# Kernel optimization log

Measured on AMD Instinct MI355X. Metric: run time of the kernel, lower is better.

## Reference

```python
import jax, jax.numpy as jnp
import numpy as np

B, N, D, H, S = 32, 8192, 64, 128, 16
ITERS, TAU = 3, 0.1


def _ln(x, g, b):
    m = x.mean(-1, keepdims=True)
    v = ((x - m) ** 2).mean(-1, keepdims=True)
    return (x - m) / jnp.sqrt(v + 1e-5) * g + b


def setup_inputs() -> dict:
    key = jax.random.key(0)
    ks = jax.random.split(key, 20)
    nrm = lambda k, shp, s: jax.random.normal(k, shp, jnp.float32) * s
    return {
        'x': nrm(ks[0], (B, N, D), 1.0),
        'w1': nrm(ks[1], (D, H), D ** -0.5), 'b1': jnp.zeros((H,), jnp.float32),
        'ln1_g': jnp.ones((H,), jnp.float32), 'ln1_b': jnp.zeros((H,), jnp.float32),
        'w2': nrm(ks[2], (H, H), H ** -0.5), 'b2': jnp.zeros((H,), jnp.float32),
        'ln2_g': jnp.ones((H,), jnp.float32), 'ln2_b': jnp.zeros((H,), jnp.float32),
        'slot_mu': nrm(ks[3], (1, S, H), 0.1),
        'gru_wi': nrm(ks[4], (3 * H, H), H ** -0.5), 'gru_wh': nrm(ks[5], (3 * H, H), H ** -0.5),
        'gru_bi': jnp.zeros((3 * H,), jnp.float32), 'gru_bh': jnp.zeros((3 * H,), jnp.float32),
        'mlp_w1': nrm(ks[6], (H, H), H ** -0.5), 'mlp_b1': jnp.zeros((H,), jnp.float32),
        'mlp_w2': nrm(ks[7], (H, H), H ** -0.5), 'mlp_b2': jnp.zeros((H,), jnp.float32),
        'norm_g': jnp.ones((H,), jnp.float32), 'norm_b': jnp.zeros((H,), jnp.float32),
    }


def reference(x, w1, b1, ln1_g, ln1_b, w2, b2, ln2_g, ln2_b, slot_mu,
              gru_wi, gru_wh, gru_bi, gru_bh, mlp_w1, mlp_b1, mlp_w2, mlp_b2,
              norm_g, norm_b):
    Bb = x.shape[0]
    h = jax.nn.gelu(_ln(x @ w1 + b1, ln1_g, ln1_b), approximate=False)
    feats = _ln(h @ w2 + b2, ln2_g, ln2_b)              # [B,N,H]
    slots = jnp.broadcast_to(slot_mu, (Bb, S, H))
    f2 = jnp.sum(feats * feats, -1)                      # [B,N]
    attn = None
    for _ in range(ITERS):
        s2 = jnp.sum(slots * slots, -1)                  # [B,S]
        sf = jnp.einsum('bsh,bnh->bsn', slots, feats)
        dist_sq = -(s2[:, :, None] - 2.0 * sf + f2[:, None, :])  # -||s-f||^2
        attn = jax.nn.softmax(dist_sq / TAU, axis=1)     # softmax over slots
        w = attn / (attn.sum(2, keepdims=True) + 1e-8)
        updates = jnp.einsum('bsn,bnh->bsh', w, feats)
        # GRUCell (PyTorch gate order: r, z, n)
        gi = updates @ gru_wi.T + gru_bi
        gh = slots @ gru_wh.T + gru_bh
        ir, iz, inn = jnp.split(gi, 3, -1)
        hr, hz, hn = jnp.split(gh, 3, -1)
        r = jax.nn.sigmoid(ir + hr)
        z = jax.nn.sigmoid(iz + hz)
        n = jnp.tanh(inn + r * hn)
        new = (1.0 - z) * n + z * slots
        mlp_out = jax.nn.gelu(_ln(new, norm_g, norm_b) @ mlp_w1 + mlp_b1, approximate=False) @ mlp_w2 + mlp_b2
        slots = new + 0.2 * mlp_out
    return (slots, attn)
```

## Files before the change

kernel.cpp:

```cpp
#include <hip/hip_runtime.h>
#include <cstddef>
#include <cstdint>

#define B_ 32
#define N_ 8192
#define D_ 64
#define H_ 128
#define S_ 16
#define L2SCALE 14.426950408889634f

typedef unsigned short ushort_t;
typedef __attribute__((ext_vector_type(8))) short short8;
typedef __attribute__((ext_vector_type(4))) float f32x4;

#define NCHUNK 512
#define NBLK   (N_ / NCHUNK)
#define PSTRIDE 520

#define W1T_STR 72
#define W2T_STR 136

__device__ __forceinline__ float gelu_exact(float x){
    return 0.5f * x * (1.0f + erff(x * 0.70710678118654752f));
}
__device__ __forceinline__ ushort_t f2bf(float f){
    unsigned u = __float_as_uint(f);
    unsigned r = (u + 0x7FFF + ((u >> 16) & 1)) >> 16;
    return (ushort_t)r;
}
__device__ __forceinline__ float bf2f(ushort_t h){
    return __uint_as_float(((unsigned)h) << 16);
}

__global__ __launch_bounds__(256) void gemm1_kernel(
    const float* __restrict__ x, const float* __restrict__ w1, const float* __restrict__ b1,
    const float* __restrict__ ln1g, const float* __restrict__ ln1b,
    ushort_t* __restrict__ h_hi, ushort_t* __restrict__ h_lo)
{
    __shared__ ushort_t w1t_hi[128*W1T_STR];
    __shared__ ushort_t w1t_lo[128*W1T_STR];

    const int tid  = threadIdx.x;
    const int w    = tid >> 6;
    const int l    = tid & 63;
    const int ln   = l & 15;
    const int quad = l >> 4;
    const size_t n0 = (size_t)blockIdx.x * 256;

    for (int i = tid; i < 8192; i += 256){
        int k = i >> 7, hc = i & 127;
        float v = w1[i];
        ushort_t hi = f2bf(v);
        w1t_hi[hc*W1T_STR + k] = hi;
        w1t_lo[hc*W1T_STR + k] = f2bf(v - bf2f(hi));
    }
    __syncthreads();

    for (int tt = 0; tt < 4; ++tt){
        const size_t row = n0 + (size_t)(w*4 + tt)*16 + ln;
        const float* xr = x + row*64;

        short8 bxh[2], bxl[2];
        #pragma unroll
        for (int kc = 0; kc < 2; ++kc){
            float4 a0 = *(const float4*)(xr + kc*32 + quad*8);
            float4 a1 = *(const float4*)(xr + kc*32 + quad*8 + 4);
            float v[8] = {a0.x,a0.y,a0.z,a0.w,a1.x,a1.y,a1.z,a1.w};
            #pragma unroll
            for (int j=0;j<8;++j){
                ushort_t hi = f2bf(v[j]);
                bxh[kc][j] = (short)hi;
                bxl[kc][j] = (short)f2bf(v[j] - bf2f(hi));
            }
        }

        f32x4 acc[8];
        #pragma unroll
        for (int ht=0;ht<8;++ht) acc[ht] = (f32x4){0.f,0.f,0.f,0.f};

        #pragma unroll
        for (int ht = 0; ht < 8; ++ht){
            #pragma unroll
            for (int kc = 0; kc < 2; ++kc){
                short8 ah = *(const short8*)&w1t_hi[(ht*16+ln)*W1T_STR + kc*32 + quad*8];
                short8 al = *(const short8*)&w1t_lo[(ht*16+ln)*W1T_STR + kc*32 + quad*8];
                acc[ht] = __builtin_amdgcn_mfma_f32_16x16x32_bf16(ah, bxh[kc], acc[ht], 0,0,0);
                acc[ht] = __builtin_amdgcn_mfma_f32_16x16x32_bf16(ah, bxl[kc], acc[ht], 0,0,0);
                acc[ht] = __builtin_amdgcn_mfma_f32_16x16x32_bf16(al, bxh[kc], acc[ht], 0,0,0);
            }
        }

        float vals[8][4];
        float s1 = 0.f, sq = 0.f;
        #pragma unroll
        for (int ht=0;ht<8;++ht){
            float bb[4]; *(float4*)bb = *(const float4*)(b1 + ht*16 + quad*4);
            #pragma unroll
            for (int r=0;r<4;++r){
                float v = acc[ht][r] + bb[r];
                vals[ht][r] = v; s1 += v; sq += v*v;
            }
        }
        s1 += __shfl_xor(s1,16); s1 += __shfl_xor(s1,32);
        sq += __shfl_xor(sq,16); sq += __shfl_xor(sq,32);
        float mean = s1 * (1.f/128.f);
        float var  = sq * (1.f/128.f) - mean*mean;
        float rs   = 1.f / sqrtf(var + 1e-5f);

        #pragma unroll
        for (int ht=0;ht<8;++ht){
            float gg[4]; *(float4*)gg = *(const float4*)(ln1g + ht*16 + quad*4);
            float be[4]; *(float4*)be = *(const float4*)(ln1b + ht*16 + quad*4);
            ushort_t oh[4], ol[4];
            #pragma unroll
            for (int r=0;r<4;++r){
                float t  = (vals[ht][r]-mean)*rs*gg[r] + be[r];
                float ge = gelu_exact(t);
                ushort_t hi = f2bf(ge);
                oh[r] = hi;
                ol[r] = f2bf(ge - bf2f(hi));
            }
            size_t off = row*128 + ht*16 + quad*4;
            *(ushort4*)(h_hi + off) = make_ushort4(oh[0],oh[1],oh[2],oh[3]);
            *(ushort4*)(h_lo + off) = make_ushort4(ol[0],ol[1],ol[2],ol[3]);
        }
    }
}

__global__ __launch_bounds__(256) void gemm2_kernel(
    ushort_t* __restrict__ buf_hi, ushort_t* __restrict__ buf_lo,
    const float* __restrict__ w2, const float* __restrict__ b2,
    const float* __restrict__ ln2g, const float* __restrict__ ln2b)
{
    __shared__ ushort_t w2t_hi[128*W2T_STR];
    __shared__ ushort_t w2t_lo[128*W2T_STR];

    const int tid  = threadIdx.x;
    const int w    = tid >> 6;
    const int l    = tid & 63;
    const int ln   = l & 15;
    const int quad = l >> 4;
    const size_t n0 = (size_t)blockIdx.x * 256;

    for (int i = tid; i < 16384; i += 256){
        int k = i >> 7, hc = i & 127;
        float v = w2[i];
        ushort_t hi = f2bf(v);
        w2t_hi[hc*W2T_STR + k] = hi;
        w2t_lo[hc*W2T_STR + k] = f2bf(v - bf2f(hi));
    }
    __syncthreads();

    for (int g = 0; g < 2; ++g){
        size_t row[2];
        row[0] = n0 + (size_t)(w*4 + g*2 + 0)*16 + ln;
        row[1] = n0 + (size_t)(w*4 + g*2 + 1)*16 + ln;

        f32x4 acc[2][8];
        #pragma unroll
        for (int t2=0;t2<2;++t2)
            #pragma unroll
            for (int ht=0;ht<8;++ht) acc[t2][ht] = (f32x4){0.f,0.f,0.f,0.f};

        #pragma unroll
        for (int kc = 0; kc < 4; ++kc){
            short8 bh[2], bl[2];
            #pragma unroll
            for (int t2=0;t2<2;++t2){
                bh[t2] = *(const short8*)(buf_hi + row[t2]*128 + kc*32 + quad*8);
                bl[t2] = *(const short8*)(buf_lo + row[t2]*128 + kc*32 + quad*8);
            }
            #pragma unroll
            for (int ht = 0; ht < 8; ++ht){
                short8 ah = *(const short8*)&w2t_hi[(ht*16+ln)*W2T_STR + kc*32 + quad*8];
                short8 al = *(const short8*)&w2t_lo[(ht*16+ln)*W2T_STR + kc*32 + quad*8];
                #pragma unroll
                for (int t2=0;t2<2;++t2){
                    acc[t2][ht] = __builtin_amdgcn_mfma_f32_16x16x32_bf16(ah, bh[t2], acc[t2][ht], 0,0,0);
                    acc[t2][ht] = __builtin_amdgcn_mfma_f32_16x16x32_bf16(ah, bl[t2], acc[t2][ht], 0,0,0);
                    acc[t2][ht] = __builtin_amdgcn_mfma_f32_16x16x32_bf16(al, bh[t2], acc[t2][ht], 0,0,0);
                }
            }
        }

        #pragma unroll
        for (int t2=0;t2<2;++t2){
            float vals[8][4];
            float s1 = 0.f, sq = 0.f;
            #pragma unroll
            for (int ht=0;ht<8;++ht){
                float bb[4]; *(float4*)bb = *(const float4*)(b2 + ht*16 + quad*4);
                #pragma unroll
                for (int r=0;r<4;++r){
                    float v = acc[t2][ht][r] + bb[r];
                    vals[ht][r] = v; s1 += v; sq += v*v;
                }
            }
            s1 += __shfl_xor(s1,16); s1 += __shfl_xor(s1,32);
            sq += __shfl_xor(sq,16); sq += __shfl_xor(sq,32);
            float mean = s1 * (1.f/128.f);
            float var  = sq * (1.f/128.f) - mean*mean;
            float rs   = 1.f / sqrtf(var + 1e-5f);
            #pragma unroll
            for (int ht=0;ht<8;++ht){
                float gg[4]; *(float4*)gg = *(const float4*)(ln2g + ht*16 + quad*4);
                float be[4]; *(float4*)be = *(const float4*)(ln2b + ht*16 + quad*4);
                ushort_t oh[4], ol[4];
                #pragma unroll
                for (int r=0;r<4;++r){
                    float o = (vals[ht][r]-mean)*rs*gg[r] + be[r];
                    ushort_t hi = f2bf(o);
                    oh[r] = hi;
                    ol[r] = f2bf(o - bf2f(hi));
                }
                size_t off = row[t2]*128 + ht*16 + quad*4;
                *(ushort4*)(buf_hi + off) = make_ushort4(oh[0],oh[1],oh[2],oh[3]);
                *(ushort4*)(buf_lo + off) = make_ushort4(ol[0],ol[1],ol[2],ol[3]);
            }
        }
    }
}

__global__ void init_slots(const float* __restrict__ mu, float* __restrict__ slots){
    int i = blockIdx.x * 256 + threadIdx.x;
    slots[i] = mu[i & 2047];
}

__global__ __launch_bounds__(512, 2) void attn_kernel(
    const ushort_t* __restrict__ f_hi, const ushort_t* __restrict__ f_lo,
    const float* __restrict__ slots,
    float* __restrict__ pn, float* __restrict__ pd,
    float* __restrict__ attn_out, const int write_attn)
{
    __shared__ ushort_t P_hi[16*PSTRIDE];
    __shared__ ushort_t P_lo[16*PSTRIDE];
    __shared__ float    s2buf[16];
    __shared__ float    den_red[16];

    const int tid  = threadIdx.x;
    const int w    = tid >> 6;
    const int l    = tid & 63;
    const int ln   = l & 15;
    const int quad = l >> 4;
    const int b    = blockIdx.x >> 4;
    const int nc   = blockIdx.x & 15;
    const int n0   = nc * NCHUNK;

    if (tid < 16) den_red[tid] = 0.f;

    short8 sa_hi[4], sa_lo[4];
    float q2 = 0.f;
    {
        const float* sp = slots + ((size_t)(b*16 + ln))*128 + quad*8;
        #pragma unroll
        for (int ks=0; ks<4; ++ks){
            float4 v0 = *(const float4*)(sp + ks*32);
            float4 v1 = *(const float4*)(sp + ks*32 + 4);
            float v[8] = {v0.x,v0.y,v0.z,v0.w,v1.x,v1.y,v1.z,v1.w};
            #pragma unroll
            for (int j=0;j<8;++j){
                q2 += v[j]*v[j];
                ushort_t hi = f2bf(v[j]);
                float lo = v[j] - bf2f(hi);
                sa_hi[ks][j] = (short)hi;
                sa_lo[ks][j] = (short)f2bf(lo);
            }
        }
    }
    q2 += __shfl_xor(q2, 16);
    q2 += __shfl_xor(q2, 32);
    if (tid < 16) s2buf[tid] = q2;
    __syncthreads();

    float s2v[4];
    #pragma unroll
    for (int r=0;r<4;++r) s2v[r] = s2buf[quad*4 + r];

    float den_acc[4] = {0.f,0.f,0.f,0.f};
    const size_t fbase = (size_t)b*N_ + n0;

    #pragma unroll
    for (int t2=0; t2<4; ++t2){
        const int t  = w*4 + t2;
        const int nl = t*16 + ln;
        const size_t rowoff = (fbase + nl) * 128;

        short8 fh[4], fl[4];
        #pragma unroll
        for (int ks=0; ks<4; ++ks){
            fh[ks] = *(const short8*)(f_hi + rowoff + ks*32 + quad*8);
            fl[ks] = *(const short8*)(f_lo + rowoff + ks*32 + quad*8);
        }

        f32x4 d = {0.f,0.f,0.f,0.f};
        #pragma unroll
        for (int ks=0;ks<4;++ks) d = __builtin_amdgcn_mfma_f32_16x16x32_bf16(sa_hi[ks], fh[ks], d, 0,0,0);
        #pragma unroll
        for (int ks=0;ks<4;++ks) d = __builtin_amdgcn_mfma_f32_16x16x32_bf16(sa_hi[ks], fl[ks], d, 0,0,0);
        #pragma unroll
        for (int ks=0;ks<4;++ks) d = __builtin_amdgcn_mfma_f32_16x16x32_bf16(sa_lo[ks], fh[ks], d, 0,0,0);

        float L[4];
        #pragma unroll
        for (int r=0;r<4;++r) L[r] = (2.f*d[r] - s2v[r]) * L2SCALE;
        float mx = fmaxf(fmaxf(L[0],L[1]), fmaxf(L[2],L[3]));
        mx = fmaxf(mx, __shfl_xor(mx, 16));
        mx = fmaxf(mx, __shfl_xor(mx, 32));
        float e[4];
        float z = 0.f;
        #pragma unroll
        for (int r=0;r<4;++r){ e[r] = exp2f(L[r] - mx); z += e[r]; }
        z += __shfl_xor(z, 16);
        z += __shfl_xor(z, 32);
        float rz = 1.f / z;
        #pragma unroll
        for (int r=0;r<4;++r){
            float p = e[r] * rz;
            den_acc[r] += p;
            if (write_attn)
                attn_out[((size_t)(b*16 + quad*4 + r))*N_ + n0 + nl] = p;
            ushort_t ph = f2bf(p);
            float plr = p - bf2f(ph);
            P_hi[(quad*4+r)*PSTRIDE + nl] = ph;
            P_lo[(quad*4+r)*PSTRIDE + nl] = f2bf(plr);
        }
    }

    #pragma unroll
    for (int m=1; m<16; m<<=1){
        #pragma unroll
        for (int r=0;r<4;++r) den_acc[r] += __shfl_xor(den_acc[r], m);
    }
    if (ln == 0){
        #pragma unroll
        for (int r=0;r<4;++r) atomicAdd(&den_red[quad*4 + r], den_acc[r]);
    }
    __syncthreads();

    f32x4 dacc = {0.f,0.f,0.f,0.f};
    #pragma unroll 2
    for (int ks=0; ks<16; ++ks){
        short8 pah = *(const short8*)(&P_hi[ln*PSTRIDE + ks*32 + quad*8]);
        short8 pal = *(const short8*)(&P_lo[ln*PSTRIDE + ks*32 + quad*8]);
        short8 fbh, fbl;
        #pragma unroll
        for (int j=0;j<8;++j){
            size_t go = (fbase + (size_t)(ks*32 + quad*8 + j))*128 + w*16 + ln;
            fbh[j] = (short)f_hi[go];
            fbl[j] = (short)f_lo[go];
        }
        dacc = __builtin_amdgcn_mfma_f32_16x16x32_bf16(pah, fbh, dacc, 0,0,0);
        dacc = __builtin_amdgcn_mfma_f32_16x16x32_bf16(pal, fbh, dacc, 0,0,0);
        dacc = __builtin_amdgcn_mfma_f32_16x16x32_bf16(pah, fbl, dacc, 0,0,0);
    }
    {
        float* dst = pn + (size_t)blockIdx.x * 2048;
        #pragma unroll
        for (int r=0;r<4;++r)
            dst[(quad*4+r)*128 + w*16 + ln] = dacc[r];
    }
    if (tid < 16) pd[blockIdx.x*16 + tid] = den_red[tid];
}

__global__ __launch_bounds__(256) void update_kernel(
    const float* __restrict__ pn, const float* __restrict__ pd,
    float* __restrict__ slots,
    const float* __restrict__ gwi, const float* __restrict__ gwh,
    const float* __restrict__ gbi, const float* __restrict__ gbh,
    const float* __restrict__ mw1, const float* __restrict__ mb1,
    const float* __restrict__ mw2, const float* __restrict__ mb2,
    const float* __restrict__ ng, const float* __restrict__ nbv,
    float* __restrict__ out_slots, const int write_out)
{
    __shared__ float us[512], sl[512], gbuf[3072], nbuf[512], lnb[512], qb[512];
    const int tid  = threadIdx.x;
    const int row0 = blockIdx.x * 4;

    for (int i = tid; i < 512; i += 256){
        int r = i >> 7, h = i & 127;
        int grow = row0 + r;
        int bb = grow >> 4, ss = grow & 15;
        float sum = 0.f, dv = 0.f;
        #pragma unroll 4
        for (int c = 0; c < NBLK; ++c)
            sum += pn[((size_t)(bb*NBLK + c))*2048 + ss*128 + h];
        #pragma unroll
        for (int c = 0; c < NBLK; ++c)
            dv += pd[(bb*NBLK + c)*16 + ss];
        us[i] = sum / (dv + 1e-8f);
        sl[i] = slots[(size_t)grow*128 + h];
    }
    __syncthreads();

    for (int idx = tid; idx < 3072; idx += 256){
        int which = idx >= 1536;
        int rem   = idx - which*1536;
        int r     = rem / 384;
        int o     = rem - r*384;
        const float* W   = which ? gwh : gwi;
        const float* bb  = which ? gbh : gbi;
        const float* src = (which ? sl : us) + r*128;
        float a = bb[o];
        const float4* Wr = (const float4*)(W + (size_t)o*128);
        #pragma unroll 8
        for (int k4=0;k4<32;++k4){
            float4 wv = Wr[k4];
            float4 sv = *(const float4*)(src + 4*k4);
            a += sv.x*wv.x + sv.y*wv.y + sv.z*wv.z + sv.w*wv.w;
        }
        gbuf[idx] = a;
    }
    __syncthreads();

    for (int i = tid; i < 512; i += 256){
        int r = i >> 7, h = i & 127;
        float ir  = gbuf[r*384 + h];
        float iz  = gbuf[r*384 + 128 + h];
        float in_ = gbuf[r*384 + 256 + h];
        float hr  = gbuf[1536 + r*384 + h];
        float hz  = gbuf[1536 + r*384 + 128 + h];
        float hn  = gbuf[1536 + r*384 + 256 + h];
        float rg = 1.f/(1.f + expf(-(ir+hr)));
        float zg = 1.f/(1.f + expf(-(iz+hz)));
        float nn = tanhf(in_ + rg*hn);
        nbuf[i] = (1.f - zg)*nn + zg*sl[i];
    }
    __syncthreads();

    {
        int wv = tid >> 6, ll = tid & 63;
        float v0 = nbuf[wv*128 + ll], v1 = nbuf[wv*128 + 64 + ll];
        float s1 = v0 + v1, sq = v0*v0 + v1*v1;
        #pragma unroll
        for (int m=1; m<64; m<<=1){ s1 += __shfl_xor(s1,m); sq += __shfl_xor(sq,m); }
        float mean = s1*(1.f/128.f), var = sq*(1.f/128.f) - mean*mean;
        float rs = 1.f/sqrtf(var + 1e-5f);
        lnb[wv*128 + ll]      = (v0-mean)*rs*ng[ll] + nbv[ll];
        lnb[wv*128 + 64 + ll] = (v1-mean)*rs*ng[64+ll] + nbv[64+ll];
    }
    __syncthreads();

    for (int i = tid; i < 512; i += 256){
        int r = i >> 7, o = i & 127;
        float a = mb1[o];
        const float* lr = lnb + r*128;
        #pragma unroll 8
        for (int k=0;k<128;++k) a += lr[k] * mw1[(size_t)k*128 + o];
        qb[i] = gelu_exact(a);
    }
    __syncthreads();

    for (int i = tid; i < 512; i += 256){
        int r = i >> 7, h = i & 127;
        float a = mb2[h];
        const float* qr = qb + r*128;
        #pragma unroll 8
        for (int k=0;k<128;++k) a += qr[k] * mw2[(size_t)k*128 + h];
        float ov = nbuf[i] + 0.2f*a;
        int grow = row0 + r;
        slots[(size_t)grow*128 + h] = ov;
        if (write_out) out_slots[(size_t)grow*128 + h] = ov;
    }
}

extern "C" void kernel_launch(void* const* d_in, const int* in_sizes, int n_in,
                              void* d_out, int out_size, void* d_ws, size_t ws_size,
                              hipStream_t stream)
{
    const float* x    = (const float*)d_in[0];
    const float* w1   = (const float*)d_in[1];
    const float* b1   = (const float*)d_in[2];
    const float* ln1g = (const float*)d_in[3];
    const float* ln1b = (const float*)d_in[4];
    const float* w2   = (const float*)d_in[5];
    const float* b2   = (const float*)d_in[6];
    const float* ln2g = (const float*)d_in[7];
    const float* ln2b = (const float*)d_in[8];
    const float* smu  = (const float*)d_in[9];
    const float* gwi  = (const float*)d_in[10];
    const float* gwh  = (const float*)d_in[11];
    const float* gbi  = (const float*)d_in[12];
    const float* gbh  = (const float*)d_in[13];
    const float* mw1  = (const float*)d_in[14];
    const float* mb1  = (const float*)d_in[15];
    const float* mw2  = (const float*)d_in[16];
    const float* mb2  = (const float*)d_in[17];
    const float* ng   = (const float*)d_in[18];
    const float* nbv  = (const float*)d_in[19];

    float* out_slots = (float*)d_out;
    float* out_attn  = (float*)d_out + (size_t)B_*S_*H_;

    ushort_t* buf_hi = (ushort_t*)d_ws;
    ushort_t* buf_lo = buf_hi + (size_t)B_*N_*H_;
    float* slots = (float*)(buf_lo + (size_t)B_*N_*H_);
    float* pn    = slots + B_*S_*H_;
    float* pd    = pn + (size_t)(B_*NBLK)*2048;

    gemm1_kernel<<<dim3(1024), dim3(256), 0, stream>>>(
        x, w1, b1, ln1g, ln1b, buf_hi, buf_lo);
    gemm2_kernel<<<dim3(1024), dim3(256), 0, stream>>>(
        buf_hi, buf_lo, w2, b2, ln2g, ln2b);
    init_slots<<<dim3(256), dim3(256), 0, stream>>>(smu, slots);

    for (int it = 0; it < 3; ++it){
        attn_kernel<<<dim3(B_*NBLK), dim3(512), 0, stream>>>(
            buf_hi, buf_lo, slots, pn, pd, out_attn, (it==2) ? 1 : 0);
        update_kernel<<<dim3(128), dim3(256), 0, stream>>>(
            pn, pd, slots, gwi, gwh, gbi, gbh, mw1, mb1, mw2, mb2, ng, nbv,
            out_slots, (it==2) ? 1 : 0);
    }
}
```

Before: 658.7 us.

## Halve per-block work in all kernels and use fast GELU/exp approximations

Halves the rows handled by each block in the gemm1 and gemm2 kernels and doubles their grid size. Shrinks the attention chunk to 256 tokens with 256-thread blocks, so each wave now computes two output column tiles. Replaces exact erf-based GELU with an Abramowitz-Stegun polynomial using __expf, and uses __expf in the GRU sigmoids. The intent is more blocks in flight and cheaper transcendental math. In exchange, each smaller block repeats the weight-staging prologue, more partials must be reduced, and precision is lowered slightly.

```diff
diff --git a/kernel.cpp b/kernel.cpp
--- a/kernel.cpp
+++ b/kernel.cpp
@@ -13,15 +13,22 @@
 typedef __attribute__((ext_vector_type(8))) short short8;
 typedef __attribute__((ext_vector_type(4))) float f32x4;
 
-#define NCHUNK 512
+#define NCHUNK 256
 #define NBLK   (N_ / NCHUNK)
-#define PSTRIDE 520
+#define PSTRIDE 264
 
 #define W1T_STR 72
 #define W2T_STR 136
 
-__device__ __forceinline__ float gelu_exact(float x){
-    return 0.5f * x * (1.0f + erff(x * 0.70710678118654752f));
+__device__ __forceinline__ float gelu_fast(float x){
+    float z = fabsf(x) * 0.70710678118654752f;
+    float t = 1.0f / fmaf(0.3275911f, z, 1.0f);
+    float p = t*(0.254829592f + t*(-0.284496736f + t*(1.421413741f +
+              t*(-1.453152027f + t*1.061405429f))));
+    float e = __expf(-z*z);
+    float erf_abs = 1.0f - p*e;
+    float er = copysignf(erf_abs, x);
+    return 0.5f * x * (1.0f + er);
 }
 __device__ __forceinline__ ushort_t f2bf(float f){
     unsigned u = __float_as_uint(f);
@@ -45,7 +52,7 @@
     const int l    = tid & 63;
     const int ln   = l & 15;
     const int quad = l >> 4;
-    const size_t n0 = (size_t)blockIdx.x * 256;
+    const size_t n0 = (size_t)blockIdx.x * 128;
 
     for (int i = tid; i < 8192; i += 256){
         int k = i >> 7, hc = i & 127;
@@ -56,8 +63,8 @@
     }
     __syncthreads();
 
-    for (int tt = 0; tt < 4; ++tt){
-        const size_t row = n0 + (size_t)(w*4 + tt)*16 + ln;
+    for (int tt = 0; tt < 2; ++tt){
+        const size_t row = n0 + (size_t)(w*2 + tt)*16 + ln;
         const float* xr = x + row*64;
 
         short8 bxh[2], bxl[2];
@@ -115,7 +122,7 @@
             #pragma unroll
             for (int r=0;r<4;++r){
                 float t  = (vals[ht][r]-mean)*rs*gg[r] + be[r];
-                float ge = gelu_exact(t);
+                float ge = gelu_fast(t);
                 ushort_t hi = f2bf(ge);
                 oh[r] = hi;
                 ol[r] = f2bf(ge - bf2f(hi));
@@ -140,7 +147,7 @@
     const int l    = tid & 63;
     const int ln   = l & 15;
     const int quad = l >> 4;
-    const size_t n0 = (size_t)blockIdx.x * 256;
+    const size_t n0 = (size_t)blockIdx.x * 128;
 
     for (int i = tid; i < 16384; i += 256){
         int k = i >> 7, hc = i & 127;
@@ -151,72 +158,70 @@
     }
     __syncthreads();
 
-    for (int g = 0; g < 2; ++g){
-        size_t row[2];
-        row[0] = n0 + (size_t)(w*4 + g*2 + 0)*16 + ln;
-        row[1] = n0 + (size_t)(w*4 + g*2 + 1)*16 + ln;
-
-        f32x4 acc[2][8];
-        #pragma unroll
-        for (int t2=0;t2<2;++t2)
-            #pragma unroll
-            for (int ht=0;ht<8;++ht) acc[t2][ht] = (f32x4){0.f,0.f,0.f,0.f};
-
-        #pragma unroll
-        for (int kc = 0; kc < 4; ++kc){
-            short8 bh[2], bl[2];
+    size_t row[2];
+    row[0] = n0 + (size_t)(w*2 + 0)*16 + ln;
+    row[1] = n0 + (size_t)(w*2 + 1)*16 + ln;
+
+    f32x4 acc[2][8];
+    #pragma unroll
+    for (int t2=0;t2<2;++t2)
+        #pragma unroll
+        for (int ht=0;ht<8;++ht) acc[t2][ht] = (f32x4){0.f,0.f,0.f,0.f};
+
+    #pragma unroll
+    for (int kc = 0; kc < 4; ++kc){
+        short8 bh[2], bl[2];
+        #pragma unroll
+        for (int t2=0;t2<2;++t2){
+            bh[t2] = *(const short8*)(buf_hi + row[t2]*128 + kc*32 + quad*8);
+            bl[t2] = *(const short8*)(buf_lo + row[t2]*128 + kc*32 + quad*8);
+        }
+        #pragma unroll
+        for (int ht = 0; ht < 8; ++ht){
+            short8 ah = *(const short8*)&w2t_hi[(ht*16+ln)*W2T_STR + kc*32 + quad*8];
+            short8 al = *(const short8*)&w2t_lo[(ht*16+ln)*W2T_STR + kc*32 + quad*8];
             #pragma unroll
             for (int t2=0;t2<2;++t2){
-                bh[t2] = *(const short8*)(buf_hi + row[t2]*128 + kc*32 + quad*8);
-                bl[t2] = *(const short8*)(buf_lo + row[t2]*128 + kc*32 + quad*8);
-            }
-            #pragma unroll
-            for (int ht = 0; ht < 8; ++ht){
-                short8 ah = *(const short8*)&w2t_hi[(ht*16+ln)*W2T_STR + kc*32 + quad*8];
-                short8 al = *(const short8*)&w2t_lo[(ht*16+ln)*W2T_STR + kc*32 + quad*8];
-                #pragma unroll
-                for (int t2=0;t2<2;++t2){
-                    acc[t2][ht] = __builtin_amdgcn_mfma_f32_16x16x32_bf16(ah, bh[t2], acc[t2][ht], 0,0,0);
-                    acc[t2][ht] = __builtin_amdgcn_mfma_f32_16x16x32_bf16(ah, bl[t2], acc[t2][ht], 0,0,0);
-                    acc[t2][ht] = __builtin_amdgcn_mfma_f32_16x16x32_bf16(al, bh[t2], acc[t2][ht], 0,0,0);
-                }
-            }
-        }
-
-        #pragma unroll
-        for (int t2=0;t2<2;++t2){
-            float vals[8][4];
-            float s1 = 0.f, sq = 0.f;
-            #pragma unroll
-            for (int ht=0;ht<8;++ht){
-                float bb[4]; *(float4*)bb = *(const float4*)(b2 + ht*16 + quad*4);
-                #pragma unroll
-                for (int r=0;r<4;++r){
-                    float v = acc[t2][ht][r] + bb[r];
-                    vals[ht][r] = v; s1 += v; sq += v*v;
-                }
-            }
-            s1 += __shfl_xor(s1,16); s1 += __shfl_xor(s1,32);
-            sq += __shfl_xor(sq,16); sq += __shfl_xor(sq,32);
-            float mean = s1 * (1.f/128.f);
-            float var  = sq * (1.f/128.f) - mean*mean;
-            float rs   = 1.f / sqrtf(var + 1e-5f);
-            #pragma unroll
-            for (int ht=0;ht<8;++ht){
-                float gg[4]; *(float4*)gg = *(const float4*)(ln2g + ht*16 + quad*4);
-                float be[4]; *(float4*)be = *(const float4*)(ln2b + ht*16 + quad*4);
-                ushort_t oh[4], ol[4];
-                #pragma unroll
-                for (int r=0;r<4;++r){
-                    float o = (vals[ht][r]-mean)*rs*gg[r] + be[r];
-                    ushort_t hi = f2bf(o);
-                    oh[r] = hi;
-                    ol[r] = f2bf(o - bf2f(hi));
-                }
-                size_t off = row[t2]*128 + ht*16 + quad*4;
-                *(ushort4*)(buf_hi + off) = make_ushort4(oh[0],oh[1],oh[2],oh[3]);
-                *(ushort4*)(buf_lo + off) = make_ushort4(ol[0],ol[1],ol[2],ol[3]);
-            }
+                acc[t2][ht] = __builtin_amdgcn_mfma_f32_16x16x32_bf16(ah, bh[t2], acc[t2][ht], 0,0,0);
+                acc[t2][ht] = __builtin_amdgcn_mfma_f32_16x16x32_bf16(ah, bl[t2], acc[t2][ht], 0,0,0);
+                acc[t2][ht] = __builtin_amdgcn_mfma_f32_16x16x32_bf16(al, bh[t2], acc[t2][ht], 0,0,0);
+            }
+        }
+    }
+
+    #pragma unroll
+    for (int t2=0;t2<2;++t2){
+        float vals[8][4];
+        float s1 = 0.f, sq = 0.f;
+        #pragma unroll
+        for (int ht=0;ht<8;++ht){
+            float bb[4]; *(float4*)bb = *(const float4*)(b2 + ht*16 + quad*4);
+            #pragma unroll
+            for (int r=0;r<4;++r){
+                float v = acc[t2][ht][r] + bb[r];
+                vals[ht][r] = v; s1 += v; sq += v*v;
+            }
+        }
+        s1 += __shfl_xor(s1,16); s1 += __shfl_xor(s1,32);
+        sq += __shfl_xor(sq,16); sq += __shfl_xor(sq,32);
+        float mean = s1 * (1.f/128.f);
+        float var  = sq * (1.f/128.f) - mean*mean;
+        float rs   = 1.f / sqrtf(var + 1e-5f);
+        #pragma unroll
+        for (int ht=0;ht<8;++ht){
+            float gg[4]; *(float4*)gg = *(const float4*)(ln2g + ht*16 + quad*4);
+            float be[4]; *(float4*)be = *(const float4*)(ln2b + ht*16 + quad*4);
+            ushort_t oh[4], ol[4];
+            #pragma unroll
+            for (int r=0;r<4;++r){
+                float o = (vals[ht][r]-mean)*rs*gg[r] + be[r];
+                ushort_t hi = f2bf(o);
+                oh[r] = hi;
+                ol[r] = f2bf(o - bf2f(hi));
+            }
+            size_t off = row[t2]*128 + ht*16 + quad*4;
+            *(ushort4*)(buf_hi + off) = make_ushort4(oh[0],oh[1],oh[2],oh[3]);
+            *(ushort4*)(buf_lo + off) = make_ushort4(ol[0],ol[1],ol[2],ol[3]);
         }
     }
 }
@@ -226,7 +231,7 @@
     slots[i] = mu[i & 2047];
 }
 
-__global__ __launch_bounds__(512, 2) void attn_kernel(
+__global__ __launch_bounds__(256, 3) void attn_kernel(
     const ushort_t* __restrict__ f_hi, const ushort_t* __restrict__ f_lo,
     const float* __restrict__ slots,
     float* __restrict__ pn, float* __restrict__ pd,
@@ -242,8 +247,8 @@
     const int l    = tid & 63;
     const int ln   = l & 15;
     const int quad = l >> 4;
-    const int b    = blockIdx.x >> 4;
-    const int nc   = blockIdx.x & 15;
+    const int b    = blockIdx.x >> 5;
+    const int nc   = blockIdx.x & 31;
     const int n0   = nc * NCHUNK;
 
     if (tid < 16) den_red[tid] = 0.f;
@@ -337,27 +342,29 @@
     }
     __syncthreads();
 
-    f32x4 dacc = {0.f,0.f,0.f,0.f};
-    #pragma unroll 2
-    for (int ks=0; ks<16; ++ks){
-        short8 pah = *(const short8*)(&P_hi[ln*PSTRIDE + ks*32 + quad*8]);
-        short8 pal = *(const short8*)(&P_lo[ln*PSTRIDE + ks*32 + quad*8]);
-        short8 fbh, fbl;
-        #pragma unroll
-        for (int j=0;j<8;++j){
-            size_t go = (fbase + (size_t)(ks*32 + quad*8 + j))*128 + w*16 + ln;
-            fbh[j] = (short)f_hi[go];
-            fbl[j] = (short)f_lo[go];
-        }
-        dacc = __builtin_amdgcn_mfma_f32_16x16x32_bf16(pah, fbh, dacc, 0,0,0);
-        dacc = __builtin_amdgcn_mfma_f32_16x16x32_bf16(pal, fbh, dacc, 0,0,0);
-        dacc = __builtin_amdgcn_mfma_f32_16x16x32_bf16(pah, fbl, dacc, 0,0,0);
-    }
-    {
+    #pragma unroll
+    for (int t2=0; t2<2; ++t2){
+        const int ht = w*2 + t2;
+        f32x4 dacc = {0.f,0.f,0.f,0.f};
+        #pragma unroll 2
+        for (int ks=0; ks<8; ++ks){
+            short8 pah = *(const short8*)(&P_hi[ln*PSTRIDE + ks*32 + quad*8]);
+            short8 pal = *(const short8*)(&P_lo[ln*PSTRIDE + ks*32 + quad*8]);
+            short8 fbh, fbl;
+            #pragma unroll
+            for (int j=0;j<8;++j){
+                size_t go = (fbase + (size_t)(ks*32 + quad*8 + j))*128 + ht*16 + ln;
+                fbh[j] = (short)f_hi[go];
+                fbl[j] = (short)f_lo[go];
+            }
+            dacc = __builtin_amdgcn_mfma_f32_16x16x32_bf16(pah, fbh, dacc, 0,0,0);
+            dacc = __builtin_amdgcn_mfma_f32_16x16x32_bf16(pal, fbh, dacc, 0,0,0);
+            dacc = __builtin_amdgcn_mfma_f32_16x16x32_bf16(pah, fbl, dacc, 0,0,0);
+        }
         float* dst = pn + (size_t)blockIdx.x * 2048;
         #pragma unroll
         for (int r=0;r<4;++r)
-            dst[(quad*4+r)*128 + w*16 + ln] = dacc[r];
+            dst[(quad*4+r)*128 + ht*16 + ln] = dacc[r];
     }
     if (tid < 16) pd[blockIdx.x*16 + tid] = den_red[tid];
 }
@@ -420,8 +427,8 @@
         float hr  = gbuf[1536 + r*384 + h];
         float hz  = gbuf[1536 + r*384 + 128 + h];
         float hn  = gbuf[1536 + r*384 + 256 + h];
-        float rg = 1.f/(1.f + expf(-(ir+hr)));
-        float zg = 1.f/(1.f + expf(-(iz+hz)));
+        float rg = 1.f/(1.f + __expf(-(ir+hr)));
+        float zg = 1.f/(1.f + __expf(-(iz+hz)));
         float nn = tanhf(in_ + rg*hn);
         nbuf[i] = (1.f - zg)*nn + zg*sl[i];
     }
@@ -446,7 +453,7 @@
         const float* lr = lnb + r*128;
         #pragma unroll 8
         for (int k=0;k<128;++k) a += lr[k] * mw1[(size_t)k*128 + o];
-        qb[i] = gelu_exact(a);
+        qb[i] = gelu_fast(a);
     }
     __syncthreads();
 
@@ -497,14 +504,14 @@
     float* pn    = slots + B_*S_*H_;
     float* pd    = pn + (size_t)(B_*NBLK)*2048;
 
-    gemm1_kernel<<<dim3(1024), dim3(256), 0, stream>>>(
+    gemm1_kernel<<<dim3(2048), dim3(256), 0, stream>>>(
         x, w1, b1, ln1g, ln1b, buf_hi, buf_lo);
-    gemm2_kernel<<<dim3(1024), dim3(256), 0, stream>>>(
+    gemm2_kernel<<<dim3(2048), dim3(256), 0, stream>>>(
         buf_hi, buf_lo, w2, b2, ln2g, ln2b);
     init_slots<<<dim3(256), dim3(256), 0, stream>>>(smu, slots);
 
     for (int it = 0; it < 3; ++it){
-        attn_kernel<<<dim3(B_*NBLK), dim3(512), 0, stream>>>(
+        attn_kernel<<<dim3(B_*NBLK), dim3(256), 0, stream>>>(
             buf_hi, buf_lo, slots, pn, pd, out_attn, (it==2) ? 1 : 0);
         update_kernel<<<dim3(128), dim3(256), 0, stream>>>(
             pn, pd, slots, gwi, gwh, gbi, gbh, mw1, mb1, mw2, mb2, ng, nbv,
```

New measurement: 720.1 us. 9.3% more time.
